# Kernel tuning notes

Hardware: AMD Instinct MI355X
Metric: run time of the kernel (lower is better)

## Reference

```python
import jax, jax.numpy as jnp
import numpy as np

N_NODES = 50000
N_EDGES = 800000
N_GRAPHS = 512
IN_FEATS = 256
HIDDEN = 128
OUT_FEATS = 128


def _lin(key, fan_in, fan_out):
    return jax.random.normal(key, (fan_in, fan_out), jnp.float32) * (1.0 / np.sqrt(fan_in))


def setup_inputs() -> dict:
    key = jax.random.key(0)
    ks = jax.random.split(key, 16)
    x = jax.random.normal(ks[0], (N_NODES, IN_FEATS), jnp.float32)
    edge_index = jax.random.randint(ks[1], (2, N_EDGES), 0, N_NODES, jnp.int32)
    batch = jnp.sort(jax.random.randint(ks[2], (N_NODES,), 0, N_GRAPHS, jnp.int32))
    return {
        "x": x,
        "edge_index": edge_index,
        "batch": batch,
        "num_graphs": N_GRAPHS,
        # TD branch GCN params
        "td_W1": _lin(ks[3], IN_FEATS, HIDDEN), "td_b1": jnp.zeros((HIDDEN,), jnp.float32),
        "td_W2": _lin(ks[4], HIDDEN, OUT_FEATS), "td_b2": jnp.zeros((OUT_FEATS,), jnp.float32),
        # BU branch GCN params
        "bu_W1": _lin(ks[5], IN_FEATS, HIDDEN), "bu_b1": jnp.zeros((HIDDEN,), jnp.float32),
        "bu_W2": _lin(ks[6], HIDDEN, OUT_FEATS), "bu_b2": jnp.zeros((OUT_FEATS,), jnp.float32),
        # proj_head: Linear(256,256) -> ReLU -> Linear(256,128)
        "pw1": _lin(ks[7], OUT_FEATS * 2, 256), "pb1": jnp.zeros((256,), jnp.float32),
        "pw2": _lin(ks[8], 256, 128), "pb2": jnp.zeros((128,), jnp.float32),
    }


def gcn_conv(h_in, W, b, src, dst, n_nodes):
    """PyG GCNConv: self-loops + symmetric normalization D^-1/2 (A+I) D^-1/2 X W + b."""
    h = h_in @ W  # [N, out]
    ones = jnp.ones(src.shape[0], h.dtype)
    deg = jax.ops.segment_sum(ones, dst, num_segments=n_nodes) + 1.0  # +1 for self-loop
    dinv = jax.lax.rsqrt(deg)  # deg >= 1 always
    norm = dinv[src] * dinv[dst]  # [E]
    agg = jax.ops.segment_sum(h[src] * norm[:, None], dst, num_segments=n_nodes)
    agg = agg + h * (dinv * dinv)[:, None]  # self-loop edge contribution
    return agg + b


def reference(x, edge_index, batch, num_graphs,
              td_W1, td_b1, td_W2, td_b2,
              bu_W1, bu_b1, bu_W2, bu_b2,
              pw1, pb1, pw2, pb2):
    n = x.shape[0]
    src, dst = edge_index[0], edge_index[1]

    def branch(W1, b1, W2, b2, s, d):
        h = jax.nn.relu(gcn_conv(x, W1, b1, s, d, n))
        # dropout is identity in eval mode
        h = gcn_conv(h, W2, b2, s, d, n)
        return jax.ops.segment_sum(h, batch, num_segments=num_graphs)  # global_add_pool

    td = branch(td_W1, td_b1, td_W2, td_b2, src, dst)
    bu = branch(bu_W1, bu_b1, bu_W2, bu_b2, dst, src)  # flipped edge_index
    h = jnp.concatenate([bu, td], axis=1)  # [G, 2*out_feats]
    h = jax.nn.relu(h @ pw1 + pb1) @ pw2 + pb2
    return h
```

## Files before the change

kernel.cpp:

```cpp
#include <hip/hip_runtime.h>

#define N_NODES 50000
#define N_PAD   50048
#define N_EDGES 800000
#define N_GRAPHS 512
#define F_IN 256
#define F_H 128
#define F_CAT 256

#define BSHIFT 9
#define NB 98
#define CAP 10240
#define EPB 3125

typedef __attribute__((ext_vector_type(8))) short short8;
typedef __attribute__((ext_vector_type(4))) float f32x4;
typedef unsigned int uint;
typedef unsigned short ushort;

static __device__ __forceinline__ ushort f2bf(float f) {
    uint u = __float_as_uint(f);
    u += 0x7FFF + ((u >> 16) & 1);
    return (ushort)(u >> 16);
}
static __device__ __forceinline__ float bflo(uint v) { return __uint_as_float(v << 16); }
static __device__ __forceinline__ float bfhi(uint v) { return __uint_as_float(v & 0xFFFF0000u); }
static __device__ __forceinline__ float bfu(ushort v) { return __uint_as_float((uint)v << 16); }

#define GLL(g, l) __builtin_amdgcn_global_load_lds( \
    (const __attribute__((address_space(1))) unsigned int*)(g), \
    (__attribute__((address_space(3))) unsigned int*)(l), 16, 0, 0)

__global__ __launch_bounds__(256) void csr_scatter_kernel(
        const int* __restrict__ ei, int* __restrict__ gcur,
        uint* __restrict__ ebuf_td, uint* __restrict__ ebuf_bu) {
    __shared__ int lcnt[256];
    __shared__ int lbase[256];
    int tid = threadIdx.x;
    lcnt[tid] = 0;
    __syncthreads();
    int e0 = blockIdx.x * EPB;
    for (int k = tid; k < EPB; k += 256) {
        int i = e0 + k;
        int s = ei[i], d = ei[N_EDGES + i];
        atomicAdd(&lcnt[d >> BSHIFT], 1);
        atomicAdd(&lcnt[128 + (s >> BSHIFT)], 1);
    }
    __syncthreads();
    if (tid < 2 * NB) {
        int dir = tid / NB, b = tid % NB;
        int c = lcnt[dir * 128 + b];
        lbase[dir * 128 + b] = c ? atomicAdd(&gcur[dir * NB + b], c) : 0;
    }
    __syncthreads();
    lcnt[tid] = 0;
    __syncthreads();
    for (int k = tid; k < EPB; k += 256) {
        int i = e0 + k;
        int s = ei[i], d = ei[N_EDGES + i];
        int bd = d >> BSHIFT, bs = s >> BSHIFT;
        int p = atomicAdd(&lcnt[bd], 1) + lbase[bd];
        ebuf_td[(size_t)bd * CAP + p] = (uint)s | ((uint)(d & 511) << 16);
        int q = atomicAdd(&lcnt[128 + bs], 1) + lbase[128 + bs];
        ebuf_bu[(size_t)bs * CAP + q] = (uint)d | ((uint)(s & 511) << 16);
    }
}

__global__ __launch_bounds__(256) void csr_build_kernel(
        const uint* __restrict__ ebuf_td, const uint* __restrict__ ebuf_bu,
        const int* __restrict__ gcur,
        int* off_td, int* off_bu, ushort* deg_td, ushort* deg_bu,
        float* dinv_td, float* dinv_bu, ushort* csr_td, ushort* csr_bu) {
    int b = blockIdx.x, dir = blockIdx.y;
    const uint* ebuf = dir ? ebuf_bu : ebuf_td;
    int* off     = dir ? off_bu : off_td;
    ushort* deg  = dir ? deg_bu : deg_td;
    float* dinv  = dir ? dinv_bu : dinv_td;
    ushort* csr  = dir ? csr_bu : csr_td;
    __shared__ int cntL[512], offL[512], sm[256];
    int tid = threadIdx.x;
    cntL[tid] = 0; cntL[tid + 256] = 0;
    __syncthreads();
    int rbeg = b * CAP;
    int rend = rbeg + gcur[dir * NB + b];
    for (int k = rbeg + tid; k < rend; k += 256)
        atomicAdd(&cntL[ebuf[k] >> 16], 1);
    __syncthreads();
    int a0 = cntL[tid * 2], a1 = cntL[tid * 2 + 1];
    int ps = a0 + a1;
    sm[tid] = ps;
    __syncthreads();
    for (int o = 1; o < 256; o <<= 1) {
        int u = (tid >= o) ? sm[tid - o] : 0;
        __syncthreads();
        sm[tid] += u;
        __syncthreads();
    }
    int excl = sm[tid] - ps;
    offL[tid * 2] = excl;
    offL[tid * 2 + 1] = excl + a0;
    __syncthreads();
    int nbase = b << BSHIFT;
#pragma unroll
    for (int j = 0; j < 2; j++) {
        int nloc = tid + j * 256;
        int n = nbase + nloc;
        if (n < N_NODES) {
            off[n] = rbeg + offL[nloc];
            int c = cntL[nloc];
            deg[n] = (ushort)c;
            dinv[n] = rsqrtf((float)c + 1.0f);
        }
    }
    if (b == NB - 1) {
        int n = N_NODES + tid;
        if (n < N_PAD) dinv[n] = 1.0f;
    }
    cntL[tid] = offL[tid];
    cntL[tid + 256] = offL[tid + 256];
    __syncthreads();
    for (int k = rbeg + tid; k < rend; k += 256) {
        uint e = ebuf[k];
        int slot = atomicAdd(&cntL[e >> 16], 1);
        csr[rbeg + slot] = (ushort)(e & 0xFFFF);
    }
}

__global__ void prep_w_kernel(const float* __restrict__ td_W1, const float* __restrict__ bu_W1,
                              const float* __restrict__ td_W2, const float* __restrict__ bu_W2,
                              ushort* __restrict__ Bt1, ushort* __restrict__ Wt2) {
    int n = blockIdx.x;
    int k = threadIdx.x;
    float w1 = (n < F_H) ? td_W1[(size_t)k * F_H + n] : bu_W1[(size_t)k * F_H + (n - F_H)];
    Bt1[(size_t)n * 256 + k] = f2bf(w1);
    if (k < 128) {
        float w2 = (n < F_H) ? bu_W2[(size_t)k * F_H + n]
                             : td_W2[(size_t)k * F_H + (n - F_H)];
        Wt2[(size_t)k * 256 + n] = f2bf(w2);
    }
}

__global__ __launch_bounds__(256) void gemm_mfma(
        const float* __restrict__ x, const ushort* __restrict__ Bt,
        ushort* __restrict__ C,
        const float* __restrict__ dinv_td, const float* __restrict__ dinv_bu) {
    __shared__ __align__(16) ushort As[128 * 32];
    __shared__ __align__(16) ushort Bs[128 * 32];
    int tid = threadIdx.x;
    int wave = tid >> 6, lane = tid & 63, quad = lane >> 4, l16 = lane & 15;
    size_t bm = (size_t)blockIdx.x * 128;
    size_t bn = (size_t)blockIdx.y * 128;
    const float* dsel = blockIdx.y ? dinv_bu : dinv_td;

    f32x4 acc[2][8];
    const f32x4 z4 = {0.f, 0.f, 0.f, 0.f};
#pragma unroll
    for (int i = 0; i < 2; i++)
#pragma unroll
        for (int j = 0; j < 8; j++) acc[i][j] = z4;

    int ar = tid >> 3;
    int akq = (tid & 7) * 4;
    int cb0 = wave * 64;
    int cb1 = 256 + wave * 64;
    int c0 = cb0 + lane, c1 = cb1 + lane;
    int r0 = c0 >> 2, s0 = (c0 & 3) * 8;
    int r1 = c1 >> 2, s1 = (c1 & 3) * 8;
    const ushort* b0p = Bt + (bn + r0) * 256 + s0;
    const ushort* b1p = Bt + (bn + r1) * 256 + s1;
    ushort* lB0 = Bs + cb0 * 8;
    ushort* lB1 = Bs + cb1 * 8;

    for (int kb = 0; kb < 8; kb++) {
        int k0 = kb * 32;
        float4 av[4];
#pragma unroll
        for (int j = 0; j < 4; j++) {
            size_t grow = bm + ar + j * 32;
            if (grow < N_NODES)
                av[j] = *(const float4*)(x + grow * F_IN + k0 + akq);
            else
                av[j] = make_float4(0.f, 0.f, 0.f, 0.f);
        }
        __syncthreads();
        GLL(b0p + k0, lB0);
        GLL(b1p + k0, lB1);
#pragma unroll
        for (int j = 0; j < 4; j++) {
            ushort4 u;
            u.x = f2bf(av[j].x); u.y = f2bf(av[j].y);
            u.z = f2bf(av[j].z); u.w = f2bf(av[j].w);
            *(ushort4*)(As + (ar + j * 32) * 32 + akq) = u;
        }
        __syncthreads();
        short8 af0 = *(const short8*)(As + (wave * 32 + l16) * 32 + quad * 8);
        short8 af1 = *(const short8*)(As + (wave * 32 + 16 + l16) * 32 + quad * 8);
#pragma unroll
        for (int ct = 0; ct < 8; ct++) {
            short8 bfr = *(const short8*)(Bs + (ct * 16 + l16) * 32 + quad * 8);
            acc[0][ct] = __builtin_amdgcn_mfma_f32_16x16x32_bf16(af0, bfr, acc[0][ct], 0, 0, 0);
            acc[1][ct] = __builtin_amdgcn_mfma_f32_16x16x32_bf16(af1, bfr, acc[1][ct], 0, 0, 0);
        }
    }
#pragma unroll
    for (int rt = 0; rt < 2; rt++) {
#pragma unroll
        for (int r = 0; r < 4; r++) {
            size_t row = bm + wave * 32 + rt * 16 + quad * 4 + r;
            float dv = dsel[row];
#pragma unroll
            for (int ct = 0; ct < 8; ct++) {
                C[row * 256 + bn + ct * 16 + l16] = f2bf(acc[rt][ct][r] * dv);
            }
        }
    }
}

static __device__ __forceinline__ void gather_node(
        const ushort* __restrict__ base, const ushort* __restrict__ csr,
        int kb, int ke, int half, float a[4]) {
    float p[4] = {0.f, 0.f, 0.f, 0.f};
    float q[4] = {0.f, 0.f, 0.f, 0.f};
    float r[4] = {0.f, 0.f, 0.f, 0.f};
    int k = kb;
    for (; k + 16 <= ke; k += 16) {
        int i0 = csr[k + half],      i1 = csr[k + 2 + half];
        int i2 = csr[k + 4 + half],  i3 = csr[k + 6 + half];
        int i4 = csr[k + 8 + half],  i5 = csr[k + 10 + half];
        int i6 = csr[k + 12 + half], i7 = csr[k + 14 + half];
        uint2 v0 = *(const uint2*)(base + (size_t)i0 * F_CAT);
        uint2 v1 = *(const uint2*)(base + (size_t)i1 * F_CAT);
        uint2 v2 = *(const uint2*)(base + (size_t)i2 * F_CAT);
        uint2 v3 = *(const uint2*)(base + (size_t)i3 * F_CAT);
        uint2 v4 = *(const uint2*)(base + (size_t)i4 * F_CAT);
        uint2 v5 = *(const uint2*)(base + (size_t)i5 * F_CAT);
        uint2 v6 = *(const uint2*)(base + (size_t)i6 * F_CAT);
        uint2 v7 = *(const uint2*)(base + (size_t)i7 * F_CAT);
        a[0] += bflo(v0.x); a[1] += bfhi(v0.x); a[2] += bflo(v0.y); a[3] += bfhi(v0.y);
        p[0] += bflo(v1.x); p[1] += bfhi(v1.x); p[2] += bflo(v1.y); p[3] += bfhi(v1.y);
        q[0] += bflo(v2.x); q[1] += bfhi(v2.x); q[2] += bflo(v2.y); q[3] += bfhi(v2.y);
        r[0] += bflo(v3.x); r[1] += bfhi(v3.x); r[2] += bflo(v3.y); r[3] += bfhi(v3.y);
        a[0] += bflo(v4.x); a[1] += bfhi(v4.x); a[2] += bflo(v4.y); a[3] += bfhi(v4.y);
        p[0] += bflo(v5.x); p[1] += bfhi(v5.x); p[2] += bflo(v5.y); p[3] += bfhi(v5.y);
        q[0] += bflo(v6.x); q[1] += bfhi(v6.x); q[2] += bflo(v6.y); q[3] += bfhi(v6.y);
        r[0] += bflo(v7.x); r[1] += bfhi(v7.x); r[2] += bflo(v7.y); r[3] += bfhi(v7.y);
    }
    for (; k + 8 <= ke; k += 8) {
        int i0 = csr[k + half],     i1 = csr[k + 2 + half];
        int i2 = csr[k + 4 + half], i3 = csr[k + 6 + half];
        uint2 v0 = *(const uint2*)(base + (size_t)i0 * F_CAT);
        uint2 v1 = *(const uint2*)(base + (size_t)i1 * F_CAT);
        uint2 v2 = *(const uint2*)(base + (size_t)i2 * F_CAT);
        uint2 v3 = *(const uint2*)(base + (size_t)i3 * F_CAT);
        a[0] += bflo(v0.x); a[1] += bfhi(v0.x); a[2] += bflo(v0.y); a[3] += bfhi(v0.y);
        p[0] += bflo(v1.x); p[1] += bfhi(v1.x); p[2] += bflo(v1.y); p[3] += bfhi(v1.y);
        q[0] += bflo(v2.x); q[1] += bfhi(v2.x); q[2] += bflo(v2.y); q[3] += bfhi(v2.y);
        r[0] += bflo(v3.x); r[1] += bfhi(v3.x); r[2] += bflo(v3.y); r[3] += bfhi(v3.y);
    }
    for (; k < ke; k += 2) {
        int kk = k + half;
        if (kk < ke) {
            uint2 v = *(const uint2*)(base + (size_t)csr[kk] * F_CAT);
            a[0] += bflo(v.x); a[1] += bfhi(v.x); a[2] += bflo(v.y); a[3] += bfhi(v.y);
        }
    }
#pragma unroll
    for (int j = 0; j < 4; j++) a[j] += (p[j] + q[j]) + r[j];
}

__global__ __launch_bounds__(256) void agg1_kernel(
        const ushort* __restrict__ linS, ushort* __restrict__ h1s,
        const ushort* __restrict__ csr_td, const int* __restrict__ off_td,
        const ushort* __restrict__ deg_td, const float* __restrict__ dinv_td,
        const ushort* __restrict__ csr_bu, const int* __restrict__ off_bu,
        const ushort* __restrict__ deg_bu, const float* __restrict__ dinv_bu,
        const float* __restrict__ b_td, const float* __restrict__ b_bu) {
    int wave = threadIdx.x >> 6, lane = threadIdx.x & 63;
    int n0 = (blockIdx.x * 2 + (wave >> 1)) * 8;
    int br = wave & 1;
    const ushort* csr = br ? csr_bu : csr_td;
    const int* off    = br ? off_bu : off_td;
    const ushort* deg = br ? deg_bu : deg_td;
    const float* dinv = br ? dinv_bu : dinv_td;
    const float* bias = br ? b_bu : b_td;
    int half = lane >> 5, l32 = lane & 31;
    int col = br * F_H + l32 * 4;
    const ushort* base = linS + col;
    int bcol = l32 * 4;
    float bs0 = bias[bcol], bs1 = bias[bcol + 1];
    float bs2 = bias[bcol + 2], bs3 = bias[bcol + 3];

#pragma unroll
    for (int j = 0; j < 8; j++) {
        int n = n0 + j;
        float a[4] = {0.f, 0.f, 0.f, 0.f};
        int kb = off[n];
        gather_node(base, csr, kb, kb + deg[n], half, a);
#pragma unroll
        for (int t = 0; t < 4; t++) a[t] += __shfl_xor(a[t], 32);
        uint2 vs = *(const uint2*)(base + (size_t)n * F_CAT);
        a[0] += bflo(vs.x); a[1] += bfhi(vs.x); a[2] += bflo(vs.y); a[3] += bfhi(vs.y);
        float dn = dinv[n];
        float o0 = fmaxf(a[0] * dn + bs0, 0.f) * dn;
        float o1 = fmaxf(a[1] * dn + bs1, 0.f) * dn;
        float o2 = fmaxf(a[2] * dn + bs2, 0.f) * dn;
        float o3 = fmaxf(a[3] * dn + bs3, 0.f) * dn;
        if (half == 0) {
            uint2 pk;
            pk.x = (uint)f2bf(o0) | ((uint)f2bf(o1) << 16);
            pk.y = (uint)f2bf(o2) | ((uint)f2bf(o3) << 16);
            *(uint2*)(h1s + (size_t)n * F_CAT + col) = pk;
        }
    }
}

__global__ __launch_bounds__(256) void agg2_pool_kernel(
        const ushort* __restrict__ h1s, float* __restrict__ pooled_pre,
        const int* __restrict__ batch,
        const ushort* __restrict__ csr_td, const int* __restrict__ off_td,
        const ushort* __restrict__ deg_td, const float* __restrict__ dinv_td,
        const ushort* __restrict__ csr_bu, const int* __restrict__ off_bu,
        const ushort* __restrict__ deg_bu, const float* __restrict__ dinv_bu) {
    int wave = threadIdx.x >> 6, lane = threadIdx.x & 63;
    int n0 = (blockIdx.x * 2 + (wave >> 1)) * 8;
    int br = wave & 1;
    const ushort* csr = br ? csr_bu : csr_td;
    const int* off    = br ? off_bu : off_td;
    const ushort* deg = br ? deg_bu : deg_td;
    const float* dinv = br ? dinv_bu : dinv_td;
    int half = lane >> 5, l32 = lane & 31;
    int col = br * F_H + l32 * 4;
    const ushort* base = h1s + col;

    float acc0 = 0.f, acc1 = 0.f, acc2 = 0.f, acc3 = 0.f;
    int gcur = batch[n0];
#pragma unroll
    for (int j = 0; j < 8; j++) {
        int n = n0 + j;
        int g = batch[n];
        if (g != gcur) {
            if (half == 0) {
                float* pp = &pooled_pre[(size_t)gcur * F_CAT + col];
                unsafeAtomicAdd(pp,     acc0);
                unsafeAtomicAdd(pp + 1, acc1);
                unsafeAtomicAdd(pp + 2, acc2);
                unsafeAtomicAdd(pp + 3, acc3);
            }
            acc0 = acc1 = acc2 = acc3 = 0.f;
            gcur = g;
        }
        float a[4] = {0.f, 0.f, 0.f, 0.f};
        int kb = off[n];
        gather_node(base, csr, kb, kb + deg[n], half, a);
#pragma unroll
        for (int t = 0; t < 4; t++) a[t] += __shfl_xor(a[t], 32);
        uint2 vs = *(const uint2*)(base + (size_t)n * F_CAT);
        a[0] += bflo(vs.x); a[1] += bfhi(vs.x); a[2] += bflo(vs.y); a[3] += bfhi(vs.y);
        float dn = dinv[n];
        acc0 += a[0] * dn;
        acc1 += a[1] * dn;
        acc2 += a[2] * dn;
        acc3 += a[3] * dn;
    }
    if (half == 0) {
        float* pp = &pooled_pre[(size_t)gcur * F_CAT + col];
        unsafeAtomicAdd(pp,     acc0);
        unsafeAtomicAdd(pp + 1, acc1);
        unsafeAtomicAdd(pp + 2, acc2);
        unsafeAtomicAdd(pp + 3, acc3);
    }
}

__global__ __launch_bounds__(256) void head_kernel(
        const float* __restrict__ pooled_pre, const int* __restrict__ batch,
        const ushort* __restrict__ Wt2,
        const float* __restrict__ td_b2, const float* __restrict__ bu_b2,
        const float* __restrict__ pw1, const float* __restrict__ pb1,
        const float* __restrict__ pw2, const float* __restrict__ pb2,
        float* __restrict__ out) {
    int g = blockIdx.x;
    int tid = threadIdx.x;
    __shared__ float row[256], z[256], hid[256];
    row[tid] = pooled_pre[(size_t)g * 256 + tid];
    int lo = 0, hi = N_NODES;
    while (lo < hi) { int m = (lo + hi) >> 1; if (batch[m] < g) lo = m + 1; else hi = m; }
    int start = lo;
    lo = start; hi = N_NODES;
    while (lo < hi) { int m = (lo + hi) >> 1; if (batch[m] < g + 1) lo = m + 1; else hi = m; }
    float cnt = (float)(lo - start);
    __syncthreads();
    const float* rsel = (tid < 128) ? (row + F_H) : row;
    float b2 = (tid < 128) ? bu_b2[tid] : td_b2[tid - F_H];
    float acc = cnt * b2;
    for (int k = 0; k < F_H; k++) acc += rsel[k] * bfu(Wt2[(size_t)k * 256 + tid]);
    z[tid] = acc;
// ... 8 lines not shown
        out[(size_t)g * 128 + tid] = o;
    }
}

extern "C" void kernel_launch(void* const* d_in, const int* in_sizes, int n_in,
                              void* d_out, int out_size, void* d_ws, size_t ws_size,
                              hipStream_t stream) {
    const float* x     = (const float*)d_in[0];
    const int*   ei    = (const int*)d_in[1];
    const int*   batch = (const int*)d_in[2];
    const float* td_W1 = (const float*)d_in[4];
    const float* td_b1 = (const float*)d_in[5];
    const float* td_W2 = (const float*)d_in[6];
    const float* td_b2 = (const float*)d_in[7];
    const float* bu_W1 = (const float*)d_in[8];
    const float* bu_b1 = (const float*)d_in[9];
    const float* bu_W2 = (const float*)d_in[10];
    const float* bu_b2 = (const float*)d_in[11];
    const float* pw1   = (const float*)d_in[12];
    const float* pb1   = (const float*)d_in[13];
    const float* pw2   = (const float*)d_in[14];
    const float* pb2   = (const float*)d_in[15];
    float* out = (float*)d_out;

    char* p = (char*)d_ws;
    auto alloc = [&](size_t bytes) { void* r = (void*)p; p += (bytes + 255) & ~(size_t)255; return r; };
    char* zreg = (char*)alloc(1024 + (size_t)N_GRAPHS * F_CAT * sizeof(float));
    int* gcur = (int*)zreg;
    float* pooled_pre = (float*)(zreg + 1024);
    uint* ebuf_td = (uint*)alloc((size_t)NB * CAP * sizeof(uint));
    uint* ebuf_bu = (uint*)alloc((size_t)NB * CAP * sizeof(uint));
    ushort* csr_td = (ushort*)alloc((size_t)NB * CAP * sizeof(ushort));
    ushort* csr_bu = (ushort*)alloc((size_t)NB * CAP * sizeof(ushort));
    int* off_td = (int*)alloc((size_t)N_NODES * sizeof(int));
    int* off_bu = (int*)alloc((size_t)N_NODES * sizeof(int));
    ushort* deg_td = (ushort*)alloc((size_t)N_NODES * sizeof(ushort));
    ushort* deg_bu = (ushort*)alloc((size_t)N_NODES * sizeof(ushort));
    float* dinv_td = (float*)alloc((size_t)N_PAD * sizeof(float));
    float* dinv_bu = (float*)alloc((size_t)N_PAD * sizeof(float));
    ushort* Bt1 = (ushort*)alloc((size_t)256 * 256 * sizeof(ushort));
    ushort* Wt2 = (ushort*)alloc((size_t)128 * 256 * sizeof(ushort));
    ushort* linb = (ushort*)alloc((size_t)N_PAD * F_CAT * sizeof(ushort));
    ushort* h1s  = (ushort*)alloc((size_t)N_PAD * F_CAT * sizeof(ushort));

    hipMemsetAsync(zreg, 0, 1024 + (size_t)N_GRAPHS * F_CAT * sizeof(float), stream);

    prep_w_kernel<<<256, 256, 0, stream>>>(td_W1, bu_W1, td_W2, bu_W2, Bt1, Wt2);

    csr_scatter_kernel<<<N_EDGES / EPB, 256, 0, stream>>>(ei, gcur, ebuf_td, ebuf_bu);
    csr_build_kernel<<<dim3(NB, 2), 256, 0, stream>>>(ebuf_td, ebuf_bu, gcur,
        off_td, off_bu, deg_td, deg_bu, dinv_td, dinv_bu, csr_td, csr_bu);

    dim3 gg(N_PAD / 128, 2);
    gemm_mfma<<<gg, 256, 0, stream>>>(x, Bt1, linb, dinv_td, dinv_bu);
    agg1_kernel<<<N_NODES / 16, 256, 0, stream>>>(linb, h1s,
        csr_td, off_td, deg_td, dinv_td, csr_bu, off_bu, deg_bu, dinv_bu, td_b1, bu_b1);

    agg2_pool_kernel<<<N_NODES / 16, 256, 0, stream>>>(h1s, pooled_pre, batch,
        csr_td, off_td, deg_td, dinv_td, csr_bu, off_bu, deg_bu, dinv_bu);

    head_kernel<<<N_GRAPHS, 256, 0, stream>>>(pooled_pre, batch, Wt2,
        td_b2, bu_b2, pw1, pb1, pw2, pb2, out);
}
```

Baseline: 346.4 us.

## Fuse GEMM with CSR scatter and bake per-edge source weights into CSR

```diff
diff --git a/kernel.cpp b/kernel.cpp
--- a/kernel.cpp
+++ b/kernel.cpp
@@ -12,6 +12,7 @@
 #define NB 98
 #define CAP 10240
 #define EPB 3125
+#define GEMM_BLOCKS 782
 
 typedef __attribute__((ext_vector_type(8))) short short8;
 typedef __attribute__((ext_vector_type(4))) float f32x4;
@@ -31,38 +32,111 @@
     (const __attribute__((address_space(1))) unsigned int*)(g), \
     (__attribute__((address_space(3))) unsigned int*)(l), 16, 0, 0)
 
-__global__ __launch_bounds__(256) void csr_scatter_kernel(
+__global__ __launch_bounds__(256) void gemm_scatter_kernel(
+        const float* __restrict__ x, const ushort* __restrict__ Bt,
+        ushort* __restrict__ C,
         const int* __restrict__ ei, int* __restrict__ gcur,
         uint* __restrict__ ebuf_td, uint* __restrict__ ebuf_bu) {
+    __shared__ __align__(16) ushort As[128 * 32];
+    __shared__ __align__(16) ushort Bs[128 * 32];
     __shared__ int lcnt[256];
     __shared__ int lbase[256];
     int tid = threadIdx.x;
-    lcnt[tid] = 0;
-    __syncthreads();
-    int e0 = blockIdx.x * EPB;
-    for (int k = tid; k < EPB; k += 256) {
-        int i = e0 + k;
-        int s = ei[i], d = ei[N_EDGES + i];
-        atomicAdd(&lcnt[d >> BSHIFT], 1);
-        atomicAdd(&lcnt[128 + (s >> BSHIFT)], 1);
-    }
-    __syncthreads();
-    if (tid < 2 * NB) {
-        int dir = tid / NB, b = tid % NB;
-        int c = lcnt[dir * 128 + b];
-        lbase[dir * 128 + b] = c ? atomicAdd(&gcur[dir * NB + b], c) : 0;
-    }
-    __syncthreads();
-    lcnt[tid] = 0;
-    __syncthreads();
-    for (int k = tid; k < EPB; k += 256) {
-        int i = e0 + k;
-        int s = ei[i], d = ei[N_EDGES + i];
-        int bd = d >> BSHIFT, bs = s >> BSHIFT;
-        int p = atomicAdd(&lcnt[bd], 1) + lbase[bd];
-        ebuf_td[(size_t)bd * CAP + p] = (uint)s | ((uint)(d & 511) << 16);
-        int q = atomicAdd(&lcnt[128 + bs], 1) + lbase[128 + bs];
-        ebuf_bu[(size_t)bs * CAP + q] = (uint)d | ((uint)(s & 511) << 16);
+
+    if (blockIdx.x < GEMM_BLOCKS) {
+        int wave = tid >> 6, lane = tid & 63, quad = lane >> 4, l16 = lane & 15;
+        size_t bm = (size_t)(blockIdx.x >> 1) * 128;
+        size_t bn = (size_t)(blockIdx.x & 1) * 128;
+
+        f32x4 acc[2][8];
+        const f32x4 z4 = {0.f, 0.f, 0.f, 0.f};
+#pragma unroll
+        for (int i = 0; i < 2; i++)
+#pragma unroll
+            for (int j = 0; j < 8; j++) acc[i][j] = z4;
+
+        int ar = tid >> 3;
+        int akq = (tid & 7) * 4;
+        int cb0 = wave * 64;
+        int cb1 = 256 + wave * 64;
+        int c0 = cb0 + lane, c1 = cb1 + lane;
+        int r0 = c0 >> 2, s0 = (c0 & 3) * 8;
+        int r1 = c1 >> 2, s1 = (c1 & 3) * 8;
+        const ushort* b0p = Bt + (bn + r0) * 256 + s0;
+        const ushort* b1p = Bt + (bn + r1) * 256 + s1;
+        ushort* lB0 = Bs + cb0 * 8;
+        ushort* lB1 = Bs + cb1 * 8;
+
+        for (int kb = 0; kb < 8; kb++) {
+            int k0 = kb * 32;
+            float4 av[4];
+#pragma unroll
+            for (int j = 0; j < 4; j++) {
+                size_t grow = bm + ar + j * 32;
+                if (grow < N_NODES)
+                    av[j] = *(const float4*)(x + grow * F_IN + k0 + akq);
+                else
+                    av[j] = make_float4(0.f, 0.f, 0.f, 0.f);
+            }
+            __syncthreads();
+            GLL(b0p + k0, lB0);
+            GLL(b1p + k0, lB1);
+#pragma unroll
+            for (int j = 0; j < 4; j++) {
+                ushort4 u;
+                u.x = f2bf(av[j].x); u.y = f2bf(av[j].y);
+                u.z = f2bf(av[j].z); u.w = f2bf(av[j].w);
+                *(ushort4*)(As + (ar + j * 32) * 32 + akq) = u;
+            }
+            __syncthreads();
+            short8 af0 = *(const short8*)(As + (wave * 32 + l16) * 32 + quad * 8);
+            short8 af1 = *(const short8*)(As + (wave * 32 + 16 + l16) * 32 + quad * 8);
+#pragma unroll
+            for (int ct = 0; ct < 8; ct++) {
+                short8 bfr = *(const short8*)(Bs + (ct * 16 + l16) * 32 + quad * 8);
+                acc[0][ct] = __builtin_amdgcn_mfma_f32_16x16x32_bf16(af0, bfr, acc[0][ct], 0, 0, 0);
+                acc[1][ct] = __builtin_amdgcn_mfma_f32_16x16x32_bf16(af1, bfr, acc[1][ct], 0, 0, 0);
+            }
+        }
+#pragma unroll
+        for (int rt = 0; rt < 2; rt++) {
+#pragma unroll
+            for (int r = 0; r < 4; r++) {
+                size_t row = bm + wave * 32 + rt * 16 + quad * 4 + r;
+#pragma unroll
+                for (int ct = 0; ct < 8; ct++) {
+                    C[row * 256 + bn + ct * 16 + l16] = f2bf(acc[rt][ct][r]);
+                }
+            }
+        }
+    } else {
+        lcnt[tid] = 0;
+        __syncthreads();
+        int e0 = (blockIdx.x - GEMM_BLOCKS) * EPB;
+        for (int k = tid; k < EPB; k += 256) {
+            int i = e0 + k;
+            int s = ei[i], d = ei[N_EDGES + i];
+            atomicAdd(&lcnt[d >> BSHIFT], 1);
+            atomicAdd(&lcnt[128 + (s >> BSHIFT)], 1);
+        }
+        __syncthreads();
+        if (tid < 2 * NB) {
+            int dir = tid / NB, b = tid % NB;
+            int c = lcnt[dir * 128 + b];
+            lbase[dir * 128 + b] = c ? atomicAdd(&gcur[dir * NB + b], c) : 0;
+        }
+        __syncthreads();
+        lcnt[tid] = 0;
+        __syncthreads();
+        for (int k = tid; k < EPB; k += 256) {
+            int i = e0 + k;
+            int s = ei[i], d = ei[N_EDGES + i];
+            int bd = d >> BSHIFT, bs = s >> BSHIFT;
+            int p = atomicAdd(&lcnt[bd], 1) + lbase[bd];
+            ebuf_td[(size_t)bd * CAP + p] = (uint)s | ((uint)(d & 511) << 16);
+            int q = atomicAdd(&lcnt[128 + bs], 1) + lbase[128 + bs];
+            ebuf_bu[(size_t)bs * CAP + q] = (uint)d | ((uint)(s & 511) << 16);
+        }
     }
 }
 
@@ -112,10 +186,6 @@
             dinv[n] = rsqrtf((float)c + 1.0f);
         }
     }
-    if (b == NB - 1) {
-        int n = N_NODES + tid;
-        if (n < N_PAD) dinv[n] = 1.0f;
-    }
     cntL[tid] = offL[tid];
     cntL[tid + 256] = offL[tid + 256];
     __syncthreads();
@@ -124,6 +194,19 @@
         int slot = atomicAdd(&cntL[e >> 16], 1);
         csr[rbeg + slot] = (ushort)(e & 0xFFFF);
     }
+}
+
+__global__ __launch_bounds__(256) void bake_kernel(
+        const ushort* __restrict__ csr_td, const ushort* __restrict__ csr_bu,
+        const float* __restrict__ dinv_td, const float* __restrict__ dinv_bu,
+        uint* __restrict__ csru_td, uint* __restrict__ csru_bu) {
+    int i = blockIdx.x * 256 + threadIdx.x;
+    uint idt = csr_td[i];
+    uint idb = csr_bu[i];
+    float wt = dinv_td[idt < N_NODES ? idt : 0];
+    float wb = dinv_bu[idb < N_NODES ? idb : 0];
+    csru_td[i] = idt | ((uint)f2bf(wt) << 16);
+    csru_bu[i] = idb | ((uint)f2bf(wb) << 16);
 }
 
 __global__ void prep_w_kernel(const float* __restrict__ td_W1, const float* __restrict__ bu_W1,
@@ -140,128 +223,73 @@
     }
 }
 
-__global__ __launch_bounds__(256) void gemm_mfma(
-        const float* __restrict__ x, const ushort* __restrict__ Bt,
-        ushort* __restrict__ C,
-        const float* __restrict__ dinv_td, const float* __restrict__ dinv_bu) {
-    __shared__ __align__(16) ushort As[128 * 32];
-    __shared__ __align__(16) ushort Bs[128 * 32];
-    int tid = threadIdx.x;
-    int wave = tid >> 6, lane = tid & 63, quad = lane >> 4, l16 = lane & 15;
-    size_t bm = (size_t)blockIdx.x * 128;
-    size_t bn = (size_t)blockIdx.y * 128;
-    const float* dsel = blockIdx.y ? dinv_bu : dinv_td;
-
-    f32x4 acc[2][8];
-    const f32x4 z4 = {0.f, 0.f, 0.f, 0.f};
-#pragma unroll
-    for (int i = 0; i < 2; i++)
-#pragma unroll
-        for (int j = 0; j < 8; j++) acc[i][j] = z4;
-
-    int ar = tid >> 3;
-    int akq = (tid & 7) * 4;
-    int cb0 = wave * 64;
-    int cb1 = 256 + wave * 64;
-    int c0 = cb0 + lane, c1 = cb1 + lane;
-    int r0 = c0 >> 2, s0 = (c0 & 3) * 8;
-    int r1 = c1 >> 2, s1 = (c1 & 3) * 8;
-    const ushort* b0p = Bt + (bn + r0) * 256 + s0;
-    const ushort* b1p = Bt + (bn + r1) * 256 + s1;
-    ushort* lB0 = Bs + cb0 * 8;
-    ushort* lB1 = Bs + cb1 * 8;
-
-    for (int kb = 0; kb < 8; kb++) {
-        int k0 = kb * 32;
-        float4 av[4];
-#pragma unroll
-        for (int j = 0; j < 4; j++) {
-            size_t grow = bm + ar + j * 32;
-            if (grow < N_NODES)
-                av[j] = *(const float4*)(x + grow * F_IN + k0 + akq);
-            else
-                av[j] = make_float4(0.f, 0.f, 0.f, 0.f);
-        }
-        __syncthreads();
-        GLL(b0p + k0, lB0);
-        GLL(b1p + k0, lB1);
-#pragma unroll
-        for (int j = 0; j < 4; j++) {
-            ushort4 u;
-            u.x = f2bf(av[j].x); u.y = f2bf(av[j].y);
-            u.z = f2bf(av[j].z); u.w = f2bf(av[j].w);
-            *(ushort4*)(As + (ar + j * 32) * 32 + akq) = u;
-        }
-        __syncthreads();
-        short8 af0 = *(const short8*)(As + (wave * 32 + l16) * 32 + quad * 8);
-        short8 af1 = *(const short8*)(As + (wave * 32 + 16 + l16) * 32 + quad * 8);
-#pragma unroll
-        for (int ct = 0; ct < 8; ct++) {
-            short8 bfr = *(const short8*)(Bs + (ct * 16 + l16) * 32 + quad * 8);
-            acc[0][ct] = __builtin_amdgcn_mfma_f32_16x16x32_bf16(af0, bfr, acc[0][ct], 0, 0, 0);
-            acc[1][ct] = __builtin_amdgcn_mfma_f32_16x16x32_bf16(af1, bfr, acc[1][ct], 0, 0, 0);
-        }
-    }
-#pragma unroll
-    for (int rt = 0; rt < 2; rt++) {
-#pragma unroll
-        for (int r = 0; r < 4; r++) {
-            size_t row = bm + wave * 32 + rt * 16 + quad * 4 + r;
-            float dv = dsel[row];
-#pragma unroll
-            for (int ct = 0; ct < 8; ct++) {
-                C[row * 256 + bn + ct * 16 + l16] = f2bf(acc[rt][ct][r] * dv);
-            }
-        }
-    }
-}
-
 static __device__ __forceinline__ void gather_node(
-        const ushort* __restrict__ base, const ushort* __restrict__ csr,
+        const ushort* __restrict__ base, const uint* __restrict__ csr,
         int kb, int ke, int half, float a[4]) {
     float p[4] = {0.f, 0.f, 0.f, 0.f};
     float q[4] = {0.f, 0.f, 0.f, 0.f};
     float r[4] = {0.f, 0.f, 0.f, 0.f};
     int k = kb;
     for (; k + 16 <= ke; k += 16) {
-        int i0 = csr[k + half],      i1 = csr[k + 2 + half];
-        int i2 = csr[k + 4 + half],  i3 = csr[k + 6 + half];
-        int i4 = csr[k + 8 + half],  i5 = csr[k + 10 + half];
-        int i6 = csr[k + 12 + half], i7 = csr[k + 14 + half];
-        uint2 v0 = *(const uint2*)(base + (size_t)i0 * F_CAT);
-        uint2 v1 = *(const uint2*)(base + (size_t)i1 * F_CAT);
-        uint2 v2 = *(const uint2*)(base + (size_t)i2 * F_CAT);
-        uint2 v3 = *(const uint2*)(base + (size_t)i3 * F_CAT);
-        uint2 v4 = *(const uint2*)(base + (size_t)i4 * F_CAT);
-        uint2 v5 = *(const uint2*)(base + (size_t)i5 * F_CAT);
-        uint2 v6 = *(const uint2*)(base + (size_t)i6 * F_CAT);
-        uint2 v7 = *(const uint2*)(base + (size_t)i7 * F_CAT);
-        a[0] += bflo(v0.x); a[1] += bfhi(v0.x); a[2] += bflo(v0.y); a[3] += bfhi(v0.y);
-        p[0] += bflo(v1.x); p[1] += bfhi(v1.x); p[2] += bflo(v1.y); p[3] += bfhi(v1.y);
-        q[0] += bflo(v2.x); q[1] += bfhi(v2.x); q[2] += bflo(v2.y); q[3] += bfhi(v2.y);
-        r[0] += bflo(v3.x); r[1] += bfhi(v3.x); r[2] += bflo(v3.y); r[3] += bfhi(v3.y);
-        a[0] += bflo(v4.x); a[1] += bfhi(v4.x); a[2] += bflo(v4.y); a[3] += bfhi(v4.y);
-        p[0] += bflo(v5.x); p[1] += bfhi(v5.x); p[2] += bflo(v5.y); p[3] += bfhi(v5.y);
-        q[0] += bflo(v6.x); q[1] += bfhi(v6.x); q[2] += bflo(v6.y); q[3] += bfhi(v6.y);
-        r[0] += bflo(v7.x); r[1] += bfhi(v7.x); r[2] += bflo(v7.y); r[3] += bfhi(v7.y);
+        uint e0 = csr[k + half],      e1 = csr[k + 2 + half];
+        uint e2 = csr[k + 4 + half],  e3 = csr[k + 6 + half];
+        uint e4 = csr[k + 8 + half],  e5 = csr[k + 10 + half];
+        uint e6 = csr[k + 12 + half], e7 = csr[k + 14 + half];
+        uint2 v0 = *(const uint2*)(base + (size_t)(e0 & 0xFFFF) * F_CAT);
+        uint2 v1 = *(const uint2*)(base + (size_t)(e1 & 0xFFFF) * F_CAT);
+        uint2 v2 = *(const uint2*)(base + (size_t)(e2 & 0xFFFF) * F_CAT);
+        uint2 v3 = *(const uint2*)(base + (size_t)(e3 & 0xFFFF) * F_CAT);
+        uint2 v4 = *(const uint2*)(base + (size_t)(e4 & 0xFFFF) * F_CAT);
+        uint2 v5 = *(const uint2*)(base + (size_t)(e5 & 0xFFFF) * F_CAT);
+        uint2 v6 = *(const uint2*)(base + (size_t)(e6 & 0xFFFF) * F_CAT);
+        uint2 v7 = *(const uint2*)(base + (size_t)(e7 & 0xFFFF) * F_CAT);
+        float w0 = bfu((ushort)(e0 >> 16)), w1 = bfu((ushort)(e1 >> 16));
+        float w2 = bfu((ushort)(e2 >> 16)), w3 = bfu((ushort)(e3 >> 16));
+        float w4 = bfu((ushort)(e4 >> 16)), w5 = bfu((ushort)(e5 >> 16));
+        float w6 = bfu((ushort)(e6 >> 16)), w7 = bfu((ushort)(e7 >> 16));
+        a[0] = fmaf(w0, bflo(v0.x), a[0]); a[1] = fmaf(w0, bfhi(v0.x), a[1]);
+        a[2] = fmaf(w0, bflo(v0.y), a[2]); a[3] = fmaf(w0, bfhi(v0.y), a[3]);
+        p[0] = fmaf(w1, bflo(v1.x), p[0]); p[1] = fmaf(w1, bfhi(v1.x), p[1]);
+        p[2] = fmaf(w1, bflo(v1.y), p[2]); p[3] = fmaf(w1, bfhi(v1.y), p[3]);
+        q[0] = fmaf(w2, bflo(v2.x), q[0]); q[1] = fmaf(w2, bfhi(v2.x), q[1]);
+        q[2] = fmaf(w2, bflo(v2.y), q[2]); q[3] = fmaf(w2, bfhi(v2.y), q[3]);
+        r[0] = fmaf(w3, bflo(v3.x), r[0]); r[1] = fmaf(w3, bfhi(v3.x), r[1]);
+        r[2] = fmaf(w3, bflo(v3.y), r[2]); r[3] = fmaf(w3, bfhi(v3.y), r[3]);
+        a[0] = fmaf(w4, bflo(v4.x), a[0]); a[1] = fmaf(w4, bfhi(v4.x), a[1]);
+        a[2] = fmaf(w4, bflo(v4.y), a[2]); a[3] = fmaf(w4, bfhi(v4.y), a[3]);
+        p[0] = fmaf(w5, bflo(v5.x), p[0]); p[1] = fmaf(w5, bfhi(v5.x), p[1]);
+        p[2] = fmaf(w5, bflo(v5.y), p[2]); p[3] = fmaf(w5, bfhi(v5.y), p[3]);
+        q[0] = fmaf(w6, bflo(v6.x), q[0]); q[1] = fmaf(w6, bfhi(v6.x), q[1]);
+        q[2] = fmaf(w6, bflo(v6.y), q[2]); q[3] = fmaf(w6, bfhi(v6.y), q[3]);
+        r[0] = fmaf(w7, bflo(v7.x), r[0]); r[1] = fmaf(w7, bfhi(v7.x), r[1]);
+        r[2] = fmaf(w7, bflo(v7.y), r[2]); r[3] = fmaf(w7, bfhi(v7.y), r[3]);
     }
     for (; k + 8 <= ke; k += 8) {
-        int i0 = csr[k + half],     i1 = csr[k + 2 + half];
-        int i2 = csr[k + 4 + half], i3 = csr[k + 6 + half];
-        uint2 v0 = *(const uint2*)(base + (size_t)i0 * F_CAT);
-        uint2 v1 = *(const uint2*)(base + (size_t)i1 * F_CAT);
-        uint2 v2 = *(const uint2*)(base + (size_t)i2 * F_CAT);
-        uint2 v3 = *(const uint2*)(base + (size_t)i3 * F_CAT);
-        a[0] += bflo(v0.x); a[1] += bfhi(v0.x); a[2] += bflo(v0.y); a[3] += bfhi(v0.y);
-        p[0] += bflo(v1.x); p[1] += bfhi(v1.x); p[2] += bflo(v1.y); p[3] += bfhi(v1.y);
-        q[0] += bflo(v2.x); q[1] += bfhi(v2.x); q[2] += bflo(v2.y); q[3] += bfhi(v2.y);
-        r[0] += bflo(v3.x); r[1] += bfhi(v3.x); r[2] += bflo(v3.y); r[3] += bfhi(v3.y);
+        uint e0 = csr[k + half],     e1 = csr[k + 2 + half];
+        uint e2 = csr[k + 4 + half], e3 = csr[k + 6 + half];
+        uint2 v0 = *(const uint2*)(base + (size_t)(e0 & 0xFFFF) * F_CAT);
+        uint2 v1 = *(const uint2*)(base + (size_t)(e1 & 0xFFFF) * F_CAT);
+        uint2 v2 = *(const uint2*)(base + (size_t)(e2 & 0xFFFF) * F_CAT);
+        uint2 v3 = *(const uint2*)(base + (size_t)(e3 & 0xFFFF) * F_CAT);
+        float w0 = bfu((ushort)(e0 >> 16)), w1 = bfu((ushort)(e1 >> 16));
+        float w2 = bfu((ushort)(e2 >> 16)), w3 = bfu((ushort)(e3 >> 16));
+        a[0] = fmaf(w0, bflo(v0.x), a[0]); a[1] = fmaf(w0, bfhi(v0.x), a[1]);
+        a[2] = fmaf(w0, bflo(v0.y), a[2]); a[3] = fmaf(w0, bfhi(v0.y), a[3]);
+        p[0] = fmaf(w1, bflo(v1.x), p[0]); p[1] = fmaf(w1, bfhi(v1.x), p[1]);
+        p[2] = fmaf(w1, bflo(v1.y), p[2]); p[3] = fmaf(w1, bfhi(v1.y), p[3]);
+        q[0] = fmaf(w2, bflo(v2.x), q[0]); q[1] = fmaf(w2, bfhi(v2.x), q[1]);
+        q[2] = fmaf(w2, bflo(v2.y), q[2]); q[3] = fmaf(w2, bfhi(v2.y), q[3]);
+        r[0] = fmaf(w3, bflo(v3.x), r[0]); r[1] = fmaf(w3, bfhi(v3.x), r[1]);
+        r[2] = fmaf(w3, bflo(v3.y), r[2]); r[3] = fmaf(w3, bfhi(v3.y), r[3]);
     }
     for (; k < ke; k += 2) {
         int kk = k + half;
         if (kk < ke) {
-            uint2 v = *(const uint2*)(base + (size_t)csr[kk] * F_CAT);
-            a[0] += bflo(v.x); a[1] += bfhi(v.x); a[2] += bflo(v.y); a[3] += bfhi(v.y);
+            uint e = csr[kk];
+            uint2 v = *(const uint2*)(base + (size_t)(e & 0xFFFF) * F_CAT);
+            float w = bfu((ushort)(e >> 16));
+            a[0] = fmaf(w, bflo(v.x), a[0]); a[1] = fmaf(w, bfhi(v.x), a[1]);
+            a[2] = fmaf(w, bflo(v.y), a[2]); a[3] = fmaf(w, bfhi(v.y), a[3]);
         }
     }
 #pragma unroll
@@ -269,23 +297,23 @@
 }
 
 __global__ __launch_bounds__(256) void agg1_kernel(
-        const ushort* __restrict__ linS, ushort* __restrict__ h1s,
-        const ushort* __restrict__ csr_td, const int* __restrict__ off_td,
+        const ushort* __restrict__ lin, ushort* __restrict__ h1,
+        const uint* __restrict__ csru_td, const int* __restrict__ off_td,
         const ushort* __restrict__ deg_td, const float* __restrict__ dinv_td,
-        const ushort* __restrict__ csr_bu, const int* __restrict__ off_bu,
+        const uint* __restrict__ csru_bu, const int* __restrict__ off_bu,
         const ushort* __restrict__ deg_bu, const float* __restrict__ dinv_bu,
         const float* __restrict__ b_td, const float* __restrict__ b_bu) {
     int wave = threadIdx.x >> 6, lane = threadIdx.x & 63;
     int n0 = (blockIdx.x * 2 + (wave >> 1)) * 8;
     int br = wave & 1;
-    const ushort* csr = br ? csr_bu : csr_td;
+    const uint* csr   = br ? csru_bu : csru_td;
     const int* off    = br ? off_bu : off_td;
     const ushort* deg = br ? deg_bu : deg_td;
     const float* dinv = br ? dinv_bu : dinv_td;
     const float* bias = br ? b_bu : b_td;
     int half = lane >> 5, l32 = lane & 31;
     int col = br * F_H + l32 * 4;
-    const ushort* base = linS + col;
+    const ushort* base = lin + col;
     int bcol = l32 * 4;
     float bs0 = bias[bcol], bs1 = bias[bcol + 1];
     float bs2 = bias[bcol + 2], bs3 = bias[bcol + 3];
@@ -298,39 +326,40 @@
         gather_node(base, csr, kb, kb + deg[n], half, a);
 #pragma unroll
         for (int t = 0; t < 4; t++) a[t] += __shfl_xor(a[t], 32);
+        float dn = dinv[n];
         uint2 vs = *(const uint2*)(base + (size_t)n * F_CAT);
-        a[0] += bflo(vs.x); a[1] += bfhi(vs.x); a[2] += bflo(vs.y); a[3] += bfhi(vs.y);
-        float dn = dinv[n];
-        float o0 = fmaxf(a[0] * dn + bs0, 0.f) * dn;
-        float o1 = fmaxf(a[1] * dn + bs1, 0.f) * dn;
-        float o2 = fmaxf(a[2] * dn + bs2, 0.f) * dn;
-        float o3 = fmaxf(a[3] * dn + bs3, 0.f) * dn;
+        a[0] = fmaf(dn, bflo(vs.x), a[0]); a[1] = fmaf(dn, bfhi(vs.x), a[1]);
+        a[2] = fmaf(dn, bflo(vs.y), a[2]); a[3] = fmaf(dn, bfhi(vs.y), a[3]);
+        float o0 = fmaxf(fmaf(a[0], dn, bs0), 0.f);
+        float o1 = fmaxf(fmaf(a[1], dn, bs1), 0.f);
+        float o2 = fmaxf(fmaf(a[2], dn, bs2), 0.f);
+        float o3 = fmaxf(fmaf(a[3], dn, bs3), 0.f);
         if (half == 0) {
             uint2 pk;
             pk.x = (uint)f2bf(o0) | ((uint)f2bf(o1) << 16);
             pk.y = (uint)f2bf(o2) | ((uint)f2bf(o3) << 16);
-            *(uint2*)(h1s + (size_t)n * F_CAT + col) = pk;
+            *(uint2*)(h1 + (size_t)n * F_CAT + col) = pk;
         }
     }
 }
 
 __global__ __launch_bounds__(256) void agg2_pool_kernel(
-        const ushort* __restrict__ h1s, float* __restrict__ pooled_pre,
+        const ushort* __restrict__ h1, float* __restrict__ pooled_pre,
         const int* __restrict__ batch,
-        const ushort* __restrict__ csr_td, const int* __restrict__ off_td,
+        const uint* __restrict__ csru_td, const int* __restrict__ off_td,
         const ushort* __restrict__ deg_td, const float* __restrict__ dinv_td,
-        const ushort* __restrict__ csr_bu, const int* __restrict__ off_bu,
+        const uint* __restrict__ csru_bu, const int* __restrict__ off_bu,
         const ushort* __restrict__ deg_bu, const float* __restrict__ dinv_bu) {
     int wave = threadIdx.x >> 6, lane = threadIdx.x & 63;
     int n0 = (blockIdx.x * 2 + (wave >> 1)) * 8;
     int br = wave & 1;
-    const ushort* csr = br ? csr_bu : csr_td;
+    const uint* csr   = br ? csru_bu : csru_td;
     const int* off    = br ? off_bu : off_td;
     const ushort* deg = br ? deg_bu : deg_td;
     const float* dinv = br ? dinv_bu : dinv_td;
     int half = lane >> 5, l32 = lane & 31;
     int col = br * F_H + l32 * 4;
-    const ushort* base = h1s + col;
+    const ushort* base = h1 + col;
 
     float acc0 = 0.f, acc1 = 0.f, acc2 = 0.f, acc3 = 0.f;
     int gcur = batch[n0];
@@ -354,13 +383,14 @@
         gather_node(base, csr, kb, kb + deg[n], half, a);
 #pragma unroll
         for (int t = 0; t < 4; t++) a[t] += __shfl_xor(a[t], 32);
+        float dn = dinv[n];
         uint2 vs = *(const uint2*)(base + (size_t)n * F_CAT);
-        a[0] += bflo(vs.x); a[1] += bfhi(vs.x); a[2] += bflo(vs.y); a[3] += bfhi(vs.y);
-        float dn = dinv[n];
-        acc0 += a[0] * dn;
-        acc1 += a[1] * dn;
-        acc2 += a[2] * dn;
-        acc3 += a[3] * dn;
+        a[0] = fmaf(dn, bflo(vs.x), a[0]); a[1] = fmaf(dn, bfhi(vs.x), a[1]);
+        a[2] = fmaf(dn, bflo(vs.y), a[2]); a[3] = fmaf(dn, bfhi(vs.y), a[3]);
+        acc0 = fmaf(a[0], dn, acc0);
+        acc1 = fmaf(a[1], dn, acc1);
+        acc2 = fmaf(a[2], dn, acc2);
+        acc3 = fmaf(a[3], dn, acc3);
     }
     if (half == 0) {
         float* pp = &pooled_pre[(size_t)gcur * F_CAT + col];
@@ -435,6 +465,8 @@
     uint* ebuf_bu = (uint*)alloc((size_t)NB * CAP * sizeof(uint));
     ushort* csr_td = (ushort*)alloc((size_t)NB * CAP * sizeof(ushort));
     ushort* csr_bu = (ushort*)alloc((size_t)NB * CAP * sizeof(ushort));
+    uint* csru_td = (uint*)alloc((size_t)NB * CAP * sizeof(uint));
+    uint* csru_bu = (uint*)alloc((size_t)NB * CAP * sizeof(uint));
     int* off_td = (int*)alloc((size_t)N_NODES * sizeof(int));
     int* off_bu = (int*)alloc((size_t)N_NODES * sizeof(int));
     ushort* deg_td = (ushort*)alloc((size_t)N_NODES * sizeof(ushort));
@@ -444,23 +476,26 @@
     ushort* Bt1 = (ushort*)alloc((size_t)256 * 256 * sizeof(ushort));
     ushort* Wt2 = (ushort*)alloc((size_t)128 * 256 * sizeof(ushort));
     ushort* linb = (ushort*)alloc((size_t)N_PAD * F_CAT * sizeof(ushort));
-    ushort* h1s  = (ushort*)alloc((size_t)N_PAD * F_CAT * sizeof(ushort));
+    ushort* h1b  = (ushort*)alloc((size_t)N_PAD * F_CAT * sizeof(ushort));
 
     hipMemsetAsync(zreg, 0, 1024 + (size_t)N_GRAPHS * F_CAT * sizeof(float), stream);
 
     prep_w_kernel<<<256, 256, 0, stream>>>(td_W1, bu_W1, td_W2, bu_W2, Bt1, Wt2);
 
-    csr_scatter_kernel<<<N_EDGES / EPB, 256, 0, stream>>>(ei, gcur, ebuf_td, ebuf_bu);
+    gemm_scatter_kernel<<<GEMM_BLOCKS + N_EDGES / EPB, 256, 0, stream>>>(
+        x, Bt1, linb, ei, gcur, ebuf_td, ebuf_bu);
+
     csr_build_kernel<<<dim3(NB, 2), 256, 0, stream>>>(ebuf_td, ebuf_bu, gcur,
         off_td, off_bu, deg_td, deg_bu, dinv_td, dinv_bu, csr_td, csr_bu);
 
-    dim3 gg(N_PAD / 128, 2);
-    gemm_mfma<<<gg, 256, 0, stream>>>(x, Bt1, linb, dinv_td, dinv_bu);
-    agg1_kernel<<<N_NODES / 16, 256, 0, stream>>>(linb, h1s,
-        csr_td, off_td, deg_td, dinv_td, csr_bu, off_bu, deg_bu, dinv_bu, td_b1, bu_b1);
-
-    agg2_pool_kernel<<<N_NODES / 16, 256, 0, stream>>>(h1s, pooled_pre, batch,
-        csr_td, off_td, deg_td, dinv_td, csr_bu, off_bu, deg_bu, dinv_bu);
+    bake_kernel<<<(NB * CAP) / 256, 256, 0, stream>>>(csr_td, csr_bu,
+        dinv_td, dinv_bu, csru_td, csru_bu);
+
+    agg1_kernel<<<N_NODES / 16, 256, 0, stream>>>(linb, h1b,
+        csru_td, off_td, deg_td, dinv_td, csru_bu, off_bu, deg_bu, dinv_bu, td_b1, bu_b1);
+
+    agg2_pool_kernel<<<N_NODES / 16, 256, 0, stream>>>(h1b, pooled_pre, batch,
+        csru_td, off_td, deg_td, dinv_td, csru_bu, off_bu, deg_bu, dinv_bu);
 
     head_kernel<<<N_GRAPHS, 256, 0, stream>>>(pooled_pre, batch, Wt2,
         td_b2, bu_b2, pw1, pb1, pw2, pb2, out);
```

Measured after the change: 372.6 us. +7.6%, slower.

## Fuse first-layer GEMM with CSR edge scatter into one heterogeneous launch

Applied to the files above, without the earlier changes.

```diff
diff --git a/kernel.cpp b/kernel.cpp
--- a/kernel.cpp
+++ b/kernel.cpp
@@ -12,6 +12,7 @@
 #define NB 98
 #define CAP 10240
 #define EPB 3125
+#define GEMM_BLOCKS 782
 
 typedef __attribute__((ext_vector_type(8))) short short8;
 typedef __attribute__((ext_vector_type(4))) float f32x4;
@@ -31,38 +32,111 @@
     (const __attribute__((address_space(1))) unsigned int*)(g), \
     (__attribute__((address_space(3))) unsigned int*)(l), 16, 0, 0)
 
-__global__ __launch_bounds__(256) void csr_scatter_kernel(
+__global__ __launch_bounds__(256) void gemm_scatter_kernel(
+        const float* __restrict__ x, const ushort* __restrict__ Bt,
+        ushort* __restrict__ C,
         const int* __restrict__ ei, int* __restrict__ gcur,
         uint* __restrict__ ebuf_td, uint* __restrict__ ebuf_bu) {
+    __shared__ __align__(16) ushort As[128 * 32];
+    __shared__ __align__(16) ushort Bs[128 * 32];
     __shared__ int lcnt[256];
     __shared__ int lbase[256];
     int tid = threadIdx.x;
-    lcnt[tid] = 0;
-    __syncthreads();
-    int e0 = blockIdx.x * EPB;
-    for (int k = tid; k < EPB; k += 256) {
-        int i = e0 + k;
-        int s = ei[i], d = ei[N_EDGES + i];
-        atomicAdd(&lcnt[d >> BSHIFT], 1);
-        atomicAdd(&lcnt[128 + (s >> BSHIFT)], 1);
-    }
-    __syncthreads();
-    if (tid < 2 * NB) {
-        int dir = tid / NB, b = tid % NB;
-        int c = lcnt[dir * 128 + b];
-        lbase[dir * 128 + b] = c ? atomicAdd(&gcur[dir * NB + b], c) : 0;
-    }
-    __syncthreads();
-    lcnt[tid] = 0;
-    __syncthreads();
-    for (int k = tid; k < EPB; k += 256) {
-        int i = e0 + k;
-        int s = ei[i], d = ei[N_EDGES + i];
-        int bd = d >> BSHIFT, bs = s >> BSHIFT;
-        int p = atomicAdd(&lcnt[bd], 1) + lbase[bd];
-        ebuf_td[(size_t)bd * CAP + p] = (uint)s | ((uint)(d & 511) << 16);
-        int q = atomicAdd(&lcnt[128 + bs], 1) + lbase[128 + bs];
-        ebuf_bu[(size_t)bs * CAP + q] = (uint)d | ((uint)(s & 511) << 16);
+
+    if (blockIdx.x < GEMM_BLOCKS) {
+        int wave = tid >> 6, lane = tid & 63, quad = lane >> 4, l16 = lane & 15;
+        size_t bm = (size_t)(blockIdx.x >> 1) * 128;
+        size_t bn = (size_t)(blockIdx.x & 1) * 128;
+
+        f32x4 acc[2][8];
+        const f32x4 z4 = {0.f, 0.f, 0.f, 0.f};
+#pragma unroll
+        for (int i = 0; i < 2; i++)
+#pragma unroll
+            for (int j = 0; j < 8; j++) acc[i][j] = z4;
+
+        int ar = tid >> 3;
+        int akq = (tid & 7) * 4;
+        int cb0 = wave * 64;
+        int cb1 = 256 + wave * 64;
+        int c0 = cb0 + lane, c1 = cb1 + lane;
+        int r0 = c0 >> 2, s0 = (c0 & 3) * 8;
+        int r1 = c1 >> 2, s1 = (c1 & 3) * 8;
+        const ushort* b0p = Bt + (bn + r0) * 256 + s0;
+        const ushort* b1p = Bt + (bn + r1) * 256 + s1;
+        ushort* lB0 = Bs + cb0 * 8;
+        ushort* lB1 = Bs + cb1 * 8;
+
+        for (int kb = 0; kb < 8; kb++) {
+            int k0 = kb * 32;
+            float4 av[4];
+#pragma unroll
+            for (int j = 0; j < 4; j++) {
+                size_t grow = bm + ar + j * 32;
+                if (grow < N_NODES)
+                    av[j] = *(const float4*)(x + grow * F_IN + k0 + akq);
+                else
+                    av[j] = make_float4(0.f, 0.f, 0.f, 0.f);
+            }
+            __syncthreads();
+            GLL(b0p + k0, lB0);
+            GLL(b1p + k0, lB1);
+#pragma unroll
+            for (int j = 0; j < 4; j++) {
+                ushort4 u;
+                u.x = f2bf(av[j].x); u.y = f2bf(av[j].y);
+                u.z = f2bf(av[j].z); u.w = f2bf(av[j].w);
+                *(ushort4*)(As + (ar + j * 32) * 32 + akq) = u;
+            }
+            __syncthreads();
+            short8 af0 = *(const short8*)(As + (wave * 32 + l16) * 32 + quad * 8);
+            short8 af1 = *(const short8*)(As + (wave * 32 + 16 + l16) * 32 + quad * 8);
+#pragma unroll
+            for (int ct = 0; ct < 8; ct++) {
+                short8 bfr = *(const short8*)(Bs + (ct * 16 + l16) * 32 + quad * 8);
+                acc[0][ct] = __builtin_amdgcn_mfma_f32_16x16x32_bf16(af0, bfr, acc[0][ct], 0, 0, 0);
+                acc[1][ct] = __builtin_amdgcn_mfma_f32_16x16x32_bf16(af1, bfr, acc[1][ct], 0, 0, 0);
+            }
+        }
+#pragma unroll
+        for (int rt = 0; rt < 2; rt++) {
+#pragma unroll
+            for (int r = 0; r < 4; r++) {
+                size_t row = bm + wave * 32 + rt * 16 + quad * 4 + r;
+#pragma unroll
+                for (int ct = 0; ct < 8; ct++) {
+                    C[row * 256 + bn + ct * 16 + l16] = f2bf(acc[rt][ct][r]);
+                }
+            }
+        }
+    } else {
+        lcnt[tid] = 0;
+        __syncthreads();
+        int e0 = (blockIdx.x - GEMM_BLOCKS) * EPB;
+        for (int k = tid; k < EPB; k += 256) {
+            int i = e0 + k;
+            int s = ei[i], d = ei[N_EDGES + i];
+            atomicAdd(&lcnt[d >> BSHIFT], 1);
+            atomicAdd(&lcnt[128 + (s >> BSHIFT)], 1);
+        }
+        __syncthreads();
+        if (tid < 2 * NB) {
+            int dir = tid / NB, b = tid % NB;
+            int c = lcnt[dir * 128 + b];
+            lbase[dir * 128 + b] = c ? atomicAdd(&gcur[dir * NB + b], c) : 0;
+        }
+        __syncthreads();
+        lcnt[tid] = 0;
+        __syncthreads();
+        for (int k = tid; k < EPB; k += 256) {
+            int i = e0 + k;
+            int s = ei[i], d = ei[N_EDGES + i];
+            int bd = d >> BSHIFT, bs = s >> BSHIFT;
+            int p = atomicAdd(&lcnt[bd], 1) + lbase[bd];
+            ebuf_td[(size_t)bd * CAP + p] = (uint)s | ((uint)(d & 511) << 16);
+            int q = atomicAdd(&lcnt[128 + bs], 1) + lbase[128 + bs];
+            ebuf_bu[(size_t)bs * CAP + q] = (uint)d | ((uint)(s & 511) << 16);
+        }
     }
 }
 
@@ -126,6 +200,22 @@
     }
 }
 
+__global__ __launch_bounds__(256) void scale_kernel(
+        ushort* __restrict__ linb,
+        const float* __restrict__ dinv_td, const float* __restrict__ dinv_bu) {
+    size_t i = (size_t)blockIdx.x * 256 + threadIdx.x;
+    int row = (int)(i >> 5);
+    int c8 = ((int)i & 31) * 8;
+    float dv = (c8 < F_H) ? dinv_td[row] : dinv_bu[row];
+    uint4 v = ((uint4*)linb)[i];
+    uint4 o;
+    o.x = (uint)f2bf(bflo(v.x) * dv) | ((uint)f2bf(bfhi(v.x) * dv) << 16);
+    o.y = (uint)f2bf(bflo(v.y) * dv) | ((uint)f2bf(bfhi(v.y) * dv) << 16);
+    o.z = (uint)f2bf(bflo(v.z) * dv) | ((uint)f2bf(bfhi(v.z) * dv) << 16);
+    o.w = (uint)f2bf(bflo(v.w) * dv) | ((uint)f2bf(bfhi(v.w) * dv) << 16);
+    ((uint4*)linb)[i] = o;
+}
+
 __global__ void prep_w_kernel(const float* __restrict__ td_W1, const float* __restrict__ bu_W1,
                               const float* __restrict__ td_W2, const float* __restrict__ bu_W2,
                               ushort* __restrict__ Bt1, ushort* __restrict__ Wt2) {
@@ -137,82 +227,6 @@
         float w2 = (n < F_H) ? bu_W2[(size_t)k * F_H + n]
                              : td_W2[(size_t)k * F_H + (n - F_H)];
         Wt2[(size_t)k * 256 + n] = f2bf(w2);
-    }
-}
-
-__global__ __launch_bounds__(256) void gemm_mfma(
-        const float* __restrict__ x, const ushort* __restrict__ Bt,
-        ushort* __restrict__ C,
-        const float* __restrict__ dinv_td, const float* __restrict__ dinv_bu) {
-    __shared__ __align__(16) ushort As[128 * 32];
-    __shared__ __align__(16) ushort Bs[128 * 32];
-    int tid = threadIdx.x;
-    int wave = tid >> 6, lane = tid & 63, quad = lane >> 4, l16 = lane & 15;
-    size_t bm = (size_t)blockIdx.x * 128;
-    size_t bn = (size_t)blockIdx.y * 128;
-    const float* dsel = blockIdx.y ? dinv_bu : dinv_td;
-
-    f32x4 acc[2][8];
-    const f32x4 z4 = {0.f, 0.f, 0.f, 0.f};
-#pragma unroll
-    for (int i = 0; i < 2; i++)
-#pragma unroll
-        for (int j = 0; j < 8; j++) acc[i][j] = z4;
-
-    int ar = tid >> 3;
-    int akq = (tid & 7) * 4;
-    int cb0 = wave * 64;
-    int cb1 = 256 + wave * 64;
-    int c0 = cb0 + lane, c1 = cb1 + lane;
-    int r0 = c0 >> 2, s0 = (c0 & 3) * 8;
-    int r1 = c1 >> 2, s1 = (c1 & 3) * 8;
-    const ushort* b0p = Bt + (bn + r0) * 256 + s0;
-    const ushort* b1p = Bt + (bn + r1) * 256 + s1;
-    ushort* lB0 = Bs + cb0 * 8;
-    ushort* lB1 = Bs + cb1 * 8;
-
-    for (int kb = 0; kb < 8; kb++) {
-        int k0 = kb * 32;
-        float4 av[4];
-#pragma unroll
-        for (int j = 0; j < 4; j++) {
-            size_t grow = bm + ar + j * 32;
-            if (grow < N_NODES)
-                av[j] = *(const float4*)(x + grow * F_IN + k0 + akq);
-            else
-                av[j] = make_float4(0.f, 0.f, 0.f, 0.f);
-        }
-        __syncthreads();
-        GLL(b0p + k0, lB0);
-        GLL(b1p + k0, lB1);
-#pragma unroll
-        for (int j = 0; j < 4; j++) {
-            ushort4 u;
-            u.x = f2bf(av[j].x); u.y = f2bf(av[j].y);
-            u.z = f2bf(av[j].z); u.w = f2bf(av[j].w);
-            *(ushort4*)(As + (ar + j * 32) * 32 + akq) = u;
-        }
-        __syncthreads();
-        short8 af0 = *(const short8*)(As + (wave * 32 + l16) * 32 + quad * 8);
-        short8 af1 = *(const short8*)(As + (wave * 32 + 16 + l16) * 32 + quad * 8);
-#pragma unroll
-        for (int ct = 0; ct < 8; ct++) {
-            short8 bfr = *(const short8*)(Bs + (ct * 16 + l16) * 32 + quad * 8);
-            acc[0][ct] = __builtin_amdgcn_mfma_f32_16x16x32_bf16(af0, bfr, acc[0][ct], 0, 0, 0);
-            acc[1][ct] = __builtin_amdgcn_mfma_f32_16x16x32_bf16(af1, bfr, acc[1][ct], 0, 0, 0);
-        }
-    }
-#pragma unroll
-    for (int rt = 0; rt < 2; rt++) {
-#pragma unroll
-        for (int r = 0; r < 4; r++) {
-            size_t row = bm + wave * 32 + rt * 16 + quad * 4 + r;
-            float dv = dsel[row];
-#pragma unroll
-            for (int ct = 0; ct < 8; ct++) {
-                C[row * 256 + bn + ct * 16 + l16] = f2bf(acc[rt][ct][r] * dv);
-            }
-        }
     }
 }
 
@@ -450,12 +464,14 @@
 
     prep_w_kernel<<<256, 256, 0, stream>>>(td_W1, bu_W1, td_W2, bu_W2, Bt1, Wt2);
 
-    csr_scatter_kernel<<<N_EDGES / EPB, 256, 0, stream>>>(ei, gcur, ebuf_td, ebuf_bu);
+    gemm_scatter_kernel<<<GEMM_BLOCKS + N_EDGES / EPB, 256, 0, stream>>>(
+        x, Bt1, linb, ei, gcur, ebuf_td, ebuf_bu);
+
     csr_build_kernel<<<dim3(NB, 2), 256, 0, stream>>>(ebuf_td, ebuf_bu, gcur,
         off_td, off_bu, deg_td, deg_bu, dinv_td, dinv_bu, csr_td, csr_bu);
 
-    dim3 gg(N_PAD / 128, 2);
-    gemm_mfma<<<gg, 256, 0, stream>>>(x, Bt1, linb, dinv_td, dinv_bu);
+    scale_kernel<<<(N_PAD * F_CAT / 8) / 256, 256, 0, stream>>>(linb, dinv_td, dinv_bu);
+
     agg1_kernel<<<N_NODES / 16, 256, 0, stream>>>(linb, h1s,
         csr_td, off_td, deg_td, dinv_td, csr_bu, off_bu, deg_bu, dinv_bu, td_b1, bu_b1);
 
```

New measurement: 349.4 us. About the same (+0.9%).
